# Kernel optimization log

Hardware: AMD Instinct MI355X
Metric: run time of the kernel (lower is better)

Reference implementation:

```python
import jax, jax.numpy as jnp
import numpy as np

EPS = 1e-12  # torch F.normalize default eps


def setup_inputs() -> dict:
    key = jax.random.key(0)
    k1, k2, k3, k4, k5 = jax.random.split(key, 5)
    N, E, D_IN, D_OUT = 100000, 1600000, 128, 128
    features = jax.random.normal(k1, (N, D_IN), dtype=jnp.float32)
    W = jax.random.normal(k2, (D_OUT, D_IN), dtype=jnp.float32) * 0.05
    b = jax.random.normal(k3, (D_OUT,), dtype=jnp.float32) * 0.05
    src = jax.random.randint(k4, (E,), 0, N, dtype=jnp.int32)
    dst = jax.random.randint(k5, (E,), 0, N, dtype=jnp.int32)
    return {"features": features, "W": W, "b": b, "src": src, "dst": dst}


def reference(features, W, b, src, dst):
    N = features.shape[0]
    # sum of features over each node's neighbors: scatter-add messages to dst
    neigh_sum = jax.ops.segment_sum(features[src], dst, num_segments=N)  # [N, D]
    total = jnp.sum(features, axis=0)  # [D]
    # non-neighbor sum (excl. self) + self feature == total - neighbor_sum
    h_NN = total[None, :] - neigh_sum  # [N, D]
    # row-wise L2 normalize (torch F.normalize dim=1)
    norm = jnp.sqrt(jnp.sum(h_NN * h_NN, axis=1, keepdims=True))
    h_norm = h_NN / jnp.maximum(norm, EPS)
    # linear: x @ W.T + b
    return h_norm @ W.T + b
```

## Files before the change

kernel.cpp:

```cpp
#include <hip/hip_runtime.h>
#include <hip/hip_bf16.h>

#define D 128

typedef __bf16 bf16_t;
typedef bf16_t bf16x8 __attribute__((ext_vector_type(8)));
typedef float  f32x4  __attribute__((ext_vector_type(4)));
typedef float  f32x2  __attribute__((ext_vector_type(2)));

__device__ __forceinline__ void atomAddF(float* p, float v) {
    unsafeAtomicAdd(p, v);
}

__device__ __forceinline__ uint2 pack_fp8x8(const float* v) {
    unsigned lo = 0, hi = 0;
    lo = __builtin_amdgcn_cvt_pk_fp8_f32(v[0], v[1], lo, false);
    lo = __builtin_amdgcn_cvt_pk_fp8_f32(v[2], v[3], lo, true);
    hi = __builtin_amdgcn_cvt_pk_fp8_f32(v[4], v[5], hi, false);
    hi = __builtin_amdgcn_cvt_pk_fp8_f32(v[6], v[7], hi, true);
    return make_uint2(lo, hi);
}

__device__ __forceinline__ void acc_fp8x8(uint2 w, float* acc) {
    f32x2 a = __builtin_amdgcn_cvt_pk_f32_fp8(w.x, false);
    f32x2 b = __builtin_amdgcn_cvt_pk_f32_fp8(w.x, true);
    f32x2 c = __builtin_amdgcn_cvt_pk_f32_fp8(w.y, false);
    f32x2 d = __builtin_amdgcn_cvt_pk_f32_fp8(w.y, true);
    acc[0] += a[0]; acc[1] += a[1]; acc[2] += b[0]; acc[3] += b[1];
    acc[4] += c[0]; acc[5] += c[1]; acc[6] += d[0]; acc[7] += d[1];
}

__global__ __launch_bounds__(256) void cvt_colsum_count_kernel(const float* __restrict__ feat,
                                                               uint2* __restrict__ featq,
                                                               float* __restrict__ total,
                                                               const int* __restrict__ dst,
                                                               int* __restrict__ bcount,
                                                               int* __restrict__ chunkhist,
                                                               long long n8, int nE, int NB,
                                                               int chunk) {
    __shared__ float red[4][16][8];
    __shared__ int hist[1024];
    int tid = threadIdx.x, lane = tid & 63, w = tid >> 6;
    for (int i = tid; i < NB; i += 256) hist[i] = 0;
    __syncthreads();
    long long G = (long long)gridDim.x * 256;
    float acc[8];
    #pragma unroll
    for (int e = 0; e < 8; ++e) acc[e] = 0.f;
    int c0 = blockIdx.x * chunk;
    int c1 = c0 + chunk; if (c1 > nE) c1 = nE;
    long long i = (long long)blockIdx.x * 256 + tid;
    int e = c0 + tid;
    while (i < n8 || e < c1) {
        if (i < n8) {
            const float4 a = *(const float4*)&feat[i * 8];
            const float4 b = *(const float4*)&feat[i * 8 + 4];
            float v[8] = {a.x, a.y, a.z, a.w, b.x, b.y, b.z, b.w};
            featq[i] = pack_fp8x8(v);
            acc[0] += a.x; acc[1] += a.y; acc[2] += a.z; acc[3] += a.w;
            acc[4] += b.x; acc[5] += b.y; acc[6] += b.z; acc[7] += b.w;
        }
        if (e < c1) atomicAdd(&hist[dst[e] >> 8], 1);
        i += G; e += 256;
    }
    #pragma unroll
    for (int k = 0; k < 8; ++k) {
        acc[k] += __shfl_xor(acc[k], 16, 64);
        acc[k] += __shfl_xor(acc[k], 32, 64);
    }
    if (lane < 16) {
        #pragma unroll
        for (int k = 0; k < 8; ++k) red[w][lane][k] = acc[k];
    }
    __syncthreads();
    if (tid < 128) {
        int cb = tid >> 3, k = tid & 7;
        float s = red[0][cb][k] + red[1][cb][k] + red[2][cb][k] + red[3][cb][k];
        atomAddF(&total[cb * 8 + k], s);
    }
    int* ch = chunkhist + (size_t)blockIdx.x * 1024;
    for (int k = tid; k < NB; k += 256) {
        int h = hist[k];
        ch[k] = h;
        if (h) atomicAdd(&bcount[k], h);
    }
}

__global__ __launch_bounds__(1024) void bscan_kernel(const int* __restrict__ bcount,
                                                     int* __restrict__ bbase,
                                                     int* __restrict__ bcur,
                                                     const float* __restrict__ W,
                                                     bf16x8* __restrict__ fragbuf,
                                                     int NB, int nE) {
    int tid = threadIdx.x, lane = tid & 63, w = tid >> 6;
    int v = (tid < NB) ? bcount[tid] : 0;
    int x = v;
    #pragma unroll
    for (int off = 1; off < 64; off <<= 1) {
        int y = __shfl_up(x, off, 64);
        if (lane >= off) x += y;
    }
    __shared__ int ws[16];
    if (lane == 63) ws[w] = x;
    __syncthreads();
    if (w == 0 && lane < 16) {
        int s = ws[lane];
        #pragma unroll
        for (int off = 1; off < 16; off <<= 1) {
            int y = __shfl_up(s, off, 64);
            if (lane >= off) s += y;
        }
        ws[lane] = s;
    }
    __syncthreads();
    int base = (w == 0) ? 0 : ws[w - 1];
    int excl = base + x - v;
    if (tid < NB) { bbase[tid] = excl; bcur[tid] = excl; }
    if (tid == 0) bbase[NB] = nE;

    for (int fidx = tid; fidx < 2048; fidx += 1024) {
        int t  = fidx >> 3, fi = fidx & 7;
        int tw = t >> 6, quad = (t >> 4) & 3, l16 = t & 15;
        int s  = fi >> 1, c = fi & 1;
        int row = tw * 32 + 16 * c + l16;
        int col = 32 * s + 8 * quad;
        const float* wp = W + (size_t)row * D + col;
        float4 wa = *(const float4*)wp;
        float4 wb = *(const float4*)(wp + 4);
        bf16x8 bf;
        bf[0] = (bf16_t)wa.x; bf[1] = (bf16_t)wa.y; bf[2] = (bf16_t)wa.z; bf[3] = (bf16_t)wa.w;
        bf[4] = (bf16_t)wb.x; bf[5] = (bf16_t)wb.y; bf[6] = (bf16_t)wb.z; bf[7] = (bf16_t)wb.w;
        fragbuf[fidx] = bf;
    }
}

__global__ __launch_bounds__(256) void bucket_scatter_kernel(const int* __restrict__ src,
                                                             const int* __restrict__ dst,
                                                             int* __restrict__ bcur,
                                                             unsigned* __restrict__ packed,
                                                             const int* __restrict__ chunkhist,
                                                             int nE, int NB, int chunk) {
    __shared__ int cur[1024];
    int tid = threadIdx.x;
    const int* ch = chunkhist + (size_t)blockIdx.x * 1024;
    for (int i = tid; i < NB; i += 256) {
        int h = ch[i];
        cur[i] = h ? atomicAdd(&bcur[i], h) : 0;
    }
    __syncthreads();
    int c0 = blockIdx.x * chunk;
    int c1 = c0 + chunk; if (c1 > nE) c1 = nE;
    for (int i = c0 + tid; i < c1; i += 256) {
        int t = dst[i];
        int b = t >> 8;
        int off = atomicAdd(&cur[b], 1);
        packed[off] = ((unsigned)(t & 255) << 17) | (unsigned)src[i];
    }
}

__global__ __launch_bounds__(1024) void fill_sort_kernel(const unsigned* __restrict__ packed,
                                                         const int* __restrict__ bbase,
                                                         int* __restrict__ ptr,
                                                         int* __restrict__ adj,
                                                         int n, int NB, int nE) {
    __shared__ int cnt[256];
    __shared__ int lcur[256];
    __shared__ int wsum[4];
    int b = blockIdx.x;
    int tid = threadIdx.x, lane = tid & 63, w = tid >> 6;
    int base = bbase[b], end = bbase[b + 1];
    if (tid < 256) cnt[tid] = 0;
    __syncthreads();
    for (int i = base + tid; i < end; i += 1024)
        atomicAdd(&cnt[packed[i] >> 17], 1);
    __syncthreads();
    int v = 0, x = 0;
    if (tid < 256) {
        v = cnt[tid];
        x = v;
        #pragma unroll
        for (int off = 1; off < 64; off <<= 1) {
            int y = __shfl_up(x, off, 64);
            if (lane >= off) x += y;
        }
        if (lane == 63) wsum[w] = x;
    }
    __syncthreads();
    if (tid < 256) {
        int wb = 0;
        for (int k = 0; k < w; ++k) wb += wsum[k];
        int excl = wb + x - v;
        int start = base + excl;
        lcur[tid] = start;
        int node = b * 256 + tid;
        if (node < n) ptr[node] = start;
    }
    if (b == NB - 1 && tid == 0) ptr[n] = nE;
    __syncthreads();
    for (int i = base + tid; i < end; i += 1024) {
        unsigned pv = packed[i];
        int j = (int)(pv >> 17);
        int pos = atomicAdd(&lcur[j], 1);
        adj[pos] = (int)(pv & 0x1FFFFu);
    }
}

__global__ __launch_bounds__(256, 4) void gather_mfma_kernel(const uint2* __restrict__ featq,
                                                             const int* __restrict__ ptr,
                                                             const int* __restrict__ adj,
                                                             const float* __restrict__ total,
                                                             const bf16x8* __restrict__ fragbuf,
                                                             const float* __restrict__ bias,
                                                             float* __restrict__ out,
                                                             int n, int ngroups) {
    __shared__ bf16_t s_hn[2][16][136];

    int tid  = threadIdx.x;
    int lane = tid & 63;
    int w    = tid >> 6;
    int quad = lane >> 4;
    int l16  = lane & 15;

    int n0 = w * 32;
    float bias0 = bias[n0 + l16];
    float bias1 = bias[n0 + 16 + l16];

    int k_node = tid >> 4;
    int d8 = (tid & 15) * 8;
    float tot8[8];
    {
        float4 ta = *(const float4*)&total[d8];
        float4 tb = *(const float4*)&total[d8 + 4];
        tot8[0] = ta.x; tot8[1] = ta.y; tot8[2] = ta.z; tot8[3] = ta.w;
        tot8[4] = tb.x; tot8[5] = tb.y; tot8[6] = tb.z; tot8[7] = tb.w;
    }

    const uint2* fb = featq + (tid & 15);
    uintptr_t fragp = (uintptr_t)(fragbuf + (size_t)tid * 8);
    int pb = 0;

    for (int g = blockIdx.x; g < ngroups; g += gridDim.x) {
        int v = g * 16 + k_node;
        bool valid = v < n;
        int p0 = valid ? ptr[v] : 0;
        int p1 = valid ? ptr[v + 1] : 0;

        float acc8[8];
        #pragma unroll
        for (int e = 0; e < 8; ++e) acc8[e] = 0.f;

        for (int p = p0; p < p1; p += 16) {
            int rem = p1 - p;
            int q = p + l16; if (q > p1 - 1) q = p1 - 1;
            int myadj = adj[q];
            uint2 f[16];
            #pragma unroll
            for (int i = 0; i < 16; ++i) {
                int idx = __shfl(myadj, (lane & 48) + i, 64);
                f[i] = fb[(size_t)idx * 16];
            }
            #pragma unroll
            for (int i = 0; i < 16; ++i) asm volatile("" :: "v"(f[i]));
            #pragma unroll
            for (int i = 0; i < 16; ++i) {
                if (i < rem) acc_fp8x8(f[i], acc8);
            }
        }

        float h8[8], ss = 0.f;
        #pragma unroll
        for (int e = 0; e < 8; ++e) {
            h8[e] = valid ? (tot8[e] - acc8[e]) : 0.f;
            ss = fmaf(h8[e], h8[e], ss);
        }
        ss += __shfl_xor(ss, 1, 64);
        ss += __shfl_xor(ss, 2, 64);
        ss += __shfl_xor(ss, 4, 64);
        ss += __shfl_xor(ss, 8, 64);
        float rinv = 1.0f / fmaxf(sqrtf(ss), 1e-12f);

        bf16x8 hv;
        #pragma unroll
        for (int e = 0; e < 8; ++e) hv[e] = (bf16_t)(h8[e] * rinv);
        *(bf16x8*)&s_hn[pb][k_node][d8] = hv;
        __syncthreads();

        uintptr_t fp_ = fragp;
        asm volatile("" : "+v"(fp_));
        const bf16x8* fg = (const bf16x8*)fp_;

        f32x4 acc0 = {0.f, 0.f, 0.f, 0.f};
        f32x4 acc1 = {0.f, 0.f, 0.f, 0.f};
        #pragma unroll
        for (int s = 0; s < 4; ++s) {
            bf16x8 a  = *(const bf16x8*)&s_hn[pb][l16][32 * s + 8 * quad];
            bf16x8 b0 = fg[2 * s];
            bf16x8 b1 = fg[2 * s + 1];
            acc0 = __builtin_amdgcn_mfma_f32_16x16x32_bf16(a, b0, acc0, 0, 0, 0);
            acc1 = __builtin_amdgcn_mfma_f32_16x16x32_bf16(a, b1, acc1, 0, 0, 0);
        }
        #pragma unroll
        for (int r = 0; r < 4; ++r) {
            int row = quad * 4 + r;
            int vr = g * 16 + row;
            if (vr < n) {
                out[(size_t)vr * D + n0 + l16]      = acc0[r] + bias0;
                out[(size_t)vr * D + n0 + 16 + l16] = acc1[r] + bias1;
            }
        }
        pb ^= 1;
    }
}

__global__ __launch_bounds__(128) void col_sum_kernel(const float* __restrict__ feat,
                                                      float* __restrict__ total, int n) {
    int d = threadIdx.x;
    float acc = 0.f;
    for (int r = blockIdx.x; r < n; r += gridDim.x)
        acc += feat[(size_t)r * D + d];
    atomAddF(&total[d], acc);
}

__global__ __launch_bounds__(256) void scatter_kernel(const float* __restrict__ feat,
                                                      const int* __restrict__ src,
                                                      const int* __restrict__ dst,
                                                      float* __restrict__ neigh, int nE) {
    long long nwork = (long long)nE * 64;
    long long stride = (long long)gridDim.x * 256;
    for (long long i = (long long)blockIdx.x * 256 + threadIdx.x; i < nwork; i += stride) {
        int e = (int)(i >> 6);
        int d2 = (int)(i & 63) * 2;
        int s = src[e], t = dst[e];
        const float2 vv = *(const float2*)&feat[(size_t)s * D + d2];
        float* p = &neigh[(size_t)t * D + d2];
        atomAddF(p + 0, vv.x);
        atomAddF(p + 1, vv.y);
    }
}

__global__ __launch_bounds__(256) void finalize_kernel(const float* __restrict__ neigh,
                                                       const float* __restrict__ total,
                                                       const float* __restrict__ W,
                                                       const float* __restrict__ bias,
                                                       float* __restrict__ out,
                                                       int n, int ngroups) {
    __shared__ __hip_bfloat16 Wt[D * D];
    __shared__ __align__(16) float hnt[2][D][4];
    __shared__ float red[2][2][4];
    int tid = threadIdx.x;
    for (int idx = tid; idx < D * D; idx += 256) {
        int j = idx & 127, dd = idx >> 7;
        Wt[idx] = __float2bfloat16(W[(size_t)j * D + dd]);
    }
    int half = tid >> 7, d = tid & 127, wih = (tid >> 6) & 1, lane = tid & 63;
    float bj = bias[d], tot = total[d];
    __syncthreads();
    for (int g = blockIdx.x; g < ngroups; g += gridDim.x) {
        int nb = g * 8 + half * 4;
        float h0=0,h1=0,h2=0,h3=0;
        if (nb+0 < n) h0 = tot - neigh[(size_t)(nb+0)*D + d];
        if (nb+1 < n) h1 = tot - neigh[(size_t)(nb+1)*D + d];
        if (nb+2 < n) h2 = tot - neigh[(size_t)(nb+2)*D + d];
        if (nb+3 < n) h3 = tot - neigh[(size_t)(nb+3)*D + d];
        float s0=h0*h0,s1=h1*h1,s2=h2*h2,s3=h3*h3;
        #pragma unroll
        for (int off = 32; off > 0; off >>= 1) {
            s0 += __shfl_xor(s0, off, 64); s1 += __shfl_xor(s1, off, 64);
            s2 += __shfl_xor(s2, off, 64); s3 += __shfl_xor(s3, off, 64);
        }
        if (lane == 0) { red[half][wih][0]=s0; red[half][wih][1]=s1; red[half][wih][2]=s2; red[half][wih][3]=s3; }
        __syncthreads();
        float rinv[4];
        #pragma unroll
        for (int k = 0; k < 4; ++k)
            rinv[k] = 1.0f / fmaxf(sqrtf(red[half][0][k] + red[half][1][k]), 1e-12f);
        hnt[half][d][0]=h0*rinv[0]; hnt[half][d][1]=h1*rinv[1];
        hnt[half][d][2]=h2*rinv[2]; hnt[half][d][3]=h3*rinv[3];
        __syncthreads();
        float a0=0,a1=0,a2=0,a3=0;
        #pragma unroll 8
        for (int dd = 0; dd < D; ++dd) {
            float4 hn4 = *(const float4*)&hnt[half][dd][0];
            float wv = __bfloat162float(Wt[dd * D + d]);
            a0 = fmaf(hn4.x, wv, a0); a1 = fmaf(hn4.y, wv, a1);
            a2 = fmaf(hn4.z, wv, a2); a3 = fmaf(hn4.w, wv, a3);
        }
        if (nb+0 < n) out[(size_t)(nb+0)*D + d] = a0 + bj;
        if (nb+1 < n) out[(size_t)(nb+1)*D + d] = a1 + bj;
        if (nb+2 < n) out[(size_t)(nb+2)*D + d] = a2 + bj;
        if (nb+3 < n) out[(size_t)(nb+3)*D + d] = a3 + bj;
        __syncthreads();
    }
}

static inline size_t align_up(size_t x, size_t a) { return (x + a - 1) & ~(a - 1); }

extern "C" void kernel_launch(void* const* d_in, const int* in_sizes, int n_in,
                              void* d_out, int out_size, void* d_ws, size_t ws_size,
                              hipStream_t stream) {
    const float* feat = (const float*)d_in[0];
    const float* W    = (const float*)d_in[1];
    const float* bias = (const float*)d_in[2];
    const int*   src  = (const int*)d_in[3];
    const int*   dst  = (const int*)d_in[4];
    float* out = (float*)d_out;

    int n  = in_sizes[0] / D;
    int nE = in_sizes[3];
    int NB = (n + 255) / 256;

    char* wsb = (char*)d_ws;
    size_t o_total  = 0;
    size_t o_bcount = 512;
    size_t o_bbase  = 4608;
    size_t o_bcur   = o_bbase + 4608;
    size_t o_chist  = align_up(o_bcur + 4096, 512);
    size_t o_frag   = o_chist + (size_t)512 * 1024 * 4;
    size_t o_ptr    = o_frag + 2048 * 16;
    size_t o_adj    = align_up(o_ptr + (size_t)4 * (n + 1), 512);
    size_t o_packed = o_adj + (size_t)4 * nE;
    size_t o_featq  = align_up(o_packed + (size_t)4 * nE, 512);
    size_t needNew  = o_featq + (size_t)n * D;

    float*    total  = (float*)(wsb + o_total);
    int*      bcount = (int*)(wsb + o_bcount);
    int*      bbase  = (int*)(wsb + o_bbase);
    int*      bcur   = (int*)(wsb + o_bcur);
    int*      chist  = (int*)(wsb + o_chist);
    bf16x8*   fragbuf= (bf16x8*)(wsb + o_frag);
    int*      ptr    = (int*)(wsb + o_ptr);
    int*      adj    = (int*)(wsb + o_adj);
    unsigned* packed = (unsigned*)(wsb + o_packed);
    uint2*    featq  = (uint2*)(wsb + o_featq);

    long long n8 = (long long)n * (D / 8);
    int ngroups16 = (n + 15) / 16;
    int grid16 = (ngroups16 + 2) / 3;
    if (grid16 > 4096) grid16 = 4096;

    bool packOK = (n <= (1 << 17)) && (NB <= 1024);

    if (ws_size >= needNew && packOK) {
        hipMemsetAsync(wsb, 0, o_bbase, stream);
        int chunk = (nE + 511) / 512;
        cvt_colsum_count_kernel<<<512, 256, 0, stream>>>(feat, featq, total, dst, bcount,
                                                         chist, n8, nE, NB, chunk);
        bscan_kernel<<<1, 1024, 0, stream>>>(bcount, bbase, bcur, W, fragbuf, NB, nE);
        bucket_scatter_kernel<<<512, 256, 0, stream>>>(src, dst, bcur, packed, chist,
                                                       nE, NB, chunk);
        fill_sort_kernel<<<NB, 1024, 0, stream>>>(packed, bbase, ptr, adj, n, NB, nE);
        gather_mfma_kernel<<<grid16, 256, 0, stream>>>(featq, ptr, adj, total, fragbuf,
                                                       bias, out, n, ngroups16);
    } else {
        float* neigh = out;
        if (ws_size >= D * sizeof(float))
            hipMemsetAsync(d_ws, 0, D * sizeof(float), stream);
        hipMemsetAsync(neigh, 0, (size_t)out_size * sizeof(float), stream);
        col_sum_kernel<<<512, 128, 0, stream>>>(feat, total, n);
        scatter_kernel<<<16384, 256, 0, stream>>>(feat, src, dst, neigh, nE);
        int ngroups = (n + 7) / 8;
        finalize_kernel<<<2048, 256, 0, stream>>>(neigh, total, W, bias, out, n, ngroups);
    }
}
```

Measured before the change: 242.8 us.

## Stage bucket sort in LDS, hold W fragments in registers, prefetch adjacency

fill_sort_kernel now copies each bucket into shared memory, sorts it there and writes adj back contiguously when the bucket fits in a fixed capacity. This replaces the scattered global writes and the second global read of packed. The gather kernel converts W into bf16 MFMA fragments held in registers instead of reading a precomputed fragbuf, so the fragment-building step disappears from bscan. The neighbor feature loads are issued with inline asm using a scalar base plus 32-bit offsets, and the next adjacency chunk is loaded before waiting on them. The extra 40KB of LDS per fill_sort block may limit occupancy, and the extra registers for W fragments may limit occupancy in the gather kernel.

```diff
diff --git a/kernel.cpp b/kernel.cpp
--- a/kernel.cpp
+++ b/kernel.cpp
@@ -2,6 +2,7 @@
 #include <hip/hip_bf16.h>
 
 #define D 128
+#define FS_CAP 5120
 
 typedef __bf16 bf16_t;
 typedef bf16_t bf16x8 __attribute__((ext_vector_type(8)));
@@ -89,8 +90,6 @@
 __global__ __launch_bounds__(1024) void bscan_kernel(const int* __restrict__ bcount,
                                                      int* __restrict__ bbase,
                                                      int* __restrict__ bcur,
-                                                     const float* __restrict__ W,
-                                                     bf16x8* __restrict__ fragbuf,
                                                      int NB, int nE) {
     int tid = threadIdx.x, lane = tid & 63, w = tid >> 6;
     int v = (tid < NB) ? bcount[tid] : 0;
@@ -117,21 +116,6 @@
     int excl = base + x - v;
     if (tid < NB) { bbase[tid] = excl; bcur[tid] = excl; }
     if (tid == 0) bbase[NB] = nE;
-
-    for (int fidx = tid; fidx < 2048; fidx += 1024) {
-        int t  = fidx >> 3, fi = fidx & 7;
-        int tw = t >> 6, quad = (t >> 4) & 3, l16 = t & 15;
-        int s  = fi >> 1, c = fi & 1;
-        int row = tw * 32 + 16 * c + l16;
-        int col = 32 * s + 8 * quad;
-        const float* wp = W + (size_t)row * D + col;
-        float4 wa = *(const float4*)wp;
-        float4 wb = *(const float4*)(wp + 4);
-        bf16x8 bf;
-        bf[0] = (bf16_t)wa.x; bf[1] = (bf16_t)wa.y; bf[2] = (bf16_t)wa.z; bf[3] = (bf16_t)wa.w;
-        bf[4] = (bf16_t)wb.x; bf[5] = (bf16_t)wb.y; bf[6] = (bf16_t)wb.z; bf[7] = (bf16_t)wb.w;
-        fragbuf[fidx] = bf;
-    }
 }
 
 __global__ __launch_bounds__(256) void bucket_scatter_kernel(const int* __restrict__ src,
@@ -166,13 +150,24 @@
     __shared__ int cnt[256];
     __shared__ int lcur[256];
     __shared__ int wsum[4];
+    __shared__ int pbuf[FS_CAP];
+    __shared__ int sbuf[FS_CAP];
     int b = blockIdx.x;
     int tid = threadIdx.x, lane = tid & 63, w = tid >> 6;
-    int base = bbase[b], end = bbase[b + 1];
+    int base = bbase[b], end = bbase[b + 1], m = end - base;
+    bool fast = (m <= FS_CAP);
     if (tid < 256) cnt[tid] = 0;
     __syncthreads();
-    for (int i = base + tid; i < end; i += 1024)
-        atomicAdd(&cnt[packed[i] >> 17], 1);
+    if (fast) {
+        for (int i = tid; i < m; i += 1024) {
+            int pv = (int)packed[base + i];
+            pbuf[i] = pv;
+            atomicAdd(&cnt[pv >> 17], 1);
+        }
+    } else {
+        for (int i = tid; i < m; i += 1024)
+            atomicAdd(&cnt[packed[base + i] >> 17], 1);
+    }
     __syncthreads();
     int v = 0, x = 0;
     if (tid < 256) {
@@ -190,18 +185,29 @@
         int wb = 0;
         for (int k = 0; k < w; ++k) wb += wsum[k];
         int excl = wb + x - v;
-        int start = base + excl;
-        lcur[tid] = start;
+        lcur[tid] = fast ? excl : base + excl;
         int node = b * 256 + tid;
-        if (node < n) ptr[node] = start;
+        if (node < n) ptr[node] = base + excl;
     }
     if (b == NB - 1 && tid == 0) ptr[n] = nE;
     __syncthreads();
-    for (int i = base + tid; i < end; i += 1024) {
-        unsigned pv = packed[i];
-        int j = (int)(pv >> 17);
-        int pos = atomicAdd(&lcur[j], 1);
-        adj[pos] = (int)(pv & 0x1FFFFu);
+    if (fast) {
+        for (int i = tid; i < m; i += 1024) {
+            int pv = pbuf[i];
+            int j = pv >> 17;
+            int pos = atomicAdd(&lcur[j], 1);
+            sbuf[pos] = pv & 0x1FFFF;
+        }
+        __syncthreads();
+        for (int i = tid; i < m; i += 1024)
+            adj[base + i] = sbuf[i];
+    } else {
+        for (int i = tid; i < m; i += 1024) {
+            int pv = (int)packed[base + i];
+            int j = pv >> 17;
+            int pos = atomicAdd(&lcur[j], 1);
+            adj[pos] = pv & 0x1FFFF;
+        }
     }
 }
 
@@ -209,7 +215,7 @@
                                                              const int* __restrict__ ptr,
                                                              const int* __restrict__ adj,
                                                              const float* __restrict__ total,
-                                                             const bf16x8* __restrict__ fragbuf,
+                                                             const float* __restrict__ W,
                                                              const float* __restrict__ bias,
                                                              float* __restrict__ out,
                                                              int n, int ngroups) {
@@ -222,6 +228,19 @@
     int l16  = lane & 15;
 
     int n0 = w * 32;
+    bf16x8 bfrag[4][2];
+    #pragma unroll
+    for (int s = 0; s < 4; ++s)
+        #pragma unroll
+        for (int c = 0; c < 2; ++c) {
+            const float* wp = W + (size_t)(n0 + 16 * c + l16) * D + 32 * s + 8 * quad;
+            float4 wa = *(const float4*)wp;
+            float4 wb = *(const float4*)(wp + 4);
+            bf16x8 bf;
+            bf[0] = (bf16_t)wa.x; bf[1] = (bf16_t)wa.y; bf[2] = (bf16_t)wa.z; bf[3] = (bf16_t)wa.w;
+            bf[4] = (bf16_t)wb.x; bf[5] = (bf16_t)wb.y; bf[6] = (bf16_t)wb.z; bf[7] = (bf16_t)wb.w;
+            bfrag[s][c] = bf;
+        }
     float bias0 = bias[n0 + l16];
     float bias1 = bias[n0 + 16 + l16];
 
@@ -235,8 +254,8 @@
         tot8[4] = tb.x; tot8[5] = tb.y; tot8[6] = tb.z; tot8[7] = tb.w;
     }
 
-    const uint2* fb = featq + (tid & 15);
-    uintptr_t fragp = (uintptr_t)(fragbuf + (size_t)tid * 8);
+    unsigned sliceoff = (unsigned)(tid & 15) * 8;
+    unsigned long long fbase = (unsigned long long)featq;
     int pb = 0;
 
     for (int g = blockIdx.x; g < ngroups; g += gridDim.x) {
@@ -249,22 +268,38 @@
         #pragma unroll
         for (int e = 0; e < 8; ++e) acc8[e] = 0.f;
 
-        for (int p = p0; p < p1; p += 16) {
+        int p = p0;
+        int myadj = 0;
+        if (p < p1) {
+            int q = p + l16; if (q > p1 - 1) q = p1 - 1;
+            myadj = adj[q];
+        }
+        for (; p < p1; p += 16) {
             int rem = p1 - p;
-            int q = p + l16; if (q > p1 - 1) q = p1 - 1;
-            int myadj = adj[q];
-            uint2 f[16];
+            unsigned voff[16];
             #pragma unroll
             for (int i = 0; i < 16; ++i) {
                 int idx = __shfl(myadj, (lane & 48) + i, 64);
-                f[i] = fb[(size_t)idx * 16];
+                voff[i] = ((unsigned)idx << 7) | sliceoff;
             }
+            uint2 f[16];
             #pragma unroll
-            for (int i = 0; i < 16; ++i) asm volatile("" :: "v"(f[i]));
+            for (int i = 0; i < 16; ++i)
+                asm volatile("global_load_dwordx2 %0, %1, %2"
+                             : "=v"(f[i]) : "v"(voff[i]), "s"(fbase));
+            int adjn = 0;
+            int pn = p + 16;
+            if (pn < p1) {
+                int q = pn + l16; if (q > p1 - 1) q = p1 - 1;
+                adjn = adj[q];
+            }
+            asm volatile("s_waitcnt vmcnt(0)" ::: "memory");
+            __builtin_amdgcn_sched_barrier(0);
             #pragma unroll
             for (int i = 0; i < 16; ++i) {
                 if (i < rem) acc_fp8x8(f[i], acc8);
             }
+            myadj = adjn;
         }
 
         float h8[8], ss = 0.f;
@@ -285,19 +320,13 @@
         *(bf16x8*)&s_hn[pb][k_node][d8] = hv;
         __syncthreads();
 
-        uintptr_t fp_ = fragp;
-        asm volatile("" : "+v"(fp_));
-        const bf16x8* fg = (const bf16x8*)fp_;
-
         f32x4 acc0 = {0.f, 0.f, 0.f, 0.f};
         f32x4 acc1 = {0.f, 0.f, 0.f, 0.f};
         #pragma unroll
         for (int s = 0; s < 4; ++s) {
-            bf16x8 a  = *(const bf16x8*)&s_hn[pb][l16][32 * s + 8 * quad];
-            bf16x8 b0 = fg[2 * s];
-            bf16x8 b1 = fg[2 * s + 1];
-            acc0 = __builtin_amdgcn_mfma_f32_16x16x32_bf16(a, b0, acc0, 0, 0, 0);
-            acc1 = __builtin_amdgcn_mfma_f32_16x16x32_bf16(a, b1, acc1, 0, 0, 0);
+            bf16x8 a = *(const bf16x8*)&s_hn[pb][l16][32 * s + 8 * quad];
+            acc0 = __builtin_amdgcn_mfma_f32_16x16x32_bf16(a, bfrag[s][0], acc0, 0, 0, 0);
+            acc1 = __builtin_amdgcn_mfma_f32_16x16x32_bf16(a, bfrag[s][1], acc1, 0, 0, 0);
         }
         #pragma unroll
         for (int r = 0; r < 4; ++r) {
@@ -415,8 +444,7 @@
     size_t o_bbase  = 4608;
     size_t o_bcur   = o_bbase + 4608;
     size_t o_chist  = align_up(o_bcur + 4096, 512);
-    size_t o_frag   = o_chist + (size_t)512 * 1024 * 4;
-    size_t o_ptr    = o_frag + 2048 * 16;
+    size_t o_ptr    = o_chist + (size_t)512 * 1024 * 4;
     size_t o_adj    = align_up(o_ptr + (size_t)4 * (n + 1), 512);
     size_t o_packed = o_adj + (size_t)4 * nE;
     size_t o_featq  = align_up(o_packed + (size_t)4 * nE, 512);
@@ -427,7 +455,6 @@
     int*      bbase  = (int*)(wsb + o_bbase);
     int*      bcur   = (int*)(wsb + o_bcur);
     int*      chist  = (int*)(wsb + o_chist);
-    bf16x8*   fragbuf= (bf16x8*)(wsb + o_frag);
     int*      ptr    = (int*)(wsb + o_ptr);
     int*      adj    = (int*)(wsb + o_adj);
     unsigned* packed = (unsigned*)(wsb + o_packed);
@@ -445,11 +472,11 @@
         int chunk = (nE + 511) / 512;
         cvt_colsum_count_kernel<<<512, 256, 0, stream>>>(feat, featq, total, dst, bcount,
                                                          chist, n8, nE, NB, chunk);
-        bscan_kernel<<<1, 1024, 0, stream>>>(bcount, bbase, bcur, W, fragbuf, NB, nE);
+        bscan_kernel<<<1, 1024, 0, stream>>>(bcount, bbase, bcur, NB, nE);
         bucket_scatter_kernel<<<512, 256, 0, stream>>>(src, dst, bcur, packed, chist,
                                                        nE, NB, chunk);
         fill_sort_kernel<<<NB, 1024, 0, stream>>>(packed, bbase, ptr, adj, n, NB, nE);
-        gather_mfma_kernel<<<grid16, 256, 0, stream>>>(featq, ptr, adj, total, fragbuf,
+        gather_mfma_kernel<<<grid16, 256, 0, stream>>>(featq, ptr, adj, total, W,
                                                        bias, out, n, ngroups16);
     } else {
         float* neigh = out;
```

After: 225.1 us. 1.08x faster.
